# Optimization experiments

Measured on AMD Instinct MI355X. Metric: run time of the kernel, lower is better.

Reference implementation:

```python
import jax, jax.numpy as jnp
import numpy as np

LN_EPS = 1e-5
MASK_FILL = -1e9


def setup_inputs() -> dict:
    key = jax.random.key(0)
    ks = jax.random.split(key, 10)
    B, L, D, H, O, K = 128, 2048, 128, 256, 128, 64
    return {
        "sequence_emb": jax.random.normal(ks[0], (B, L, D), jnp.float32),
        "mask": jax.random.randint(ks[1], (B, L), 0, 2, jnp.int32),
        "target_emb": jax.random.normal(ks[2], (B, D), jnp.float32),
        "pos_table": jax.random.normal(ks[3], (10000, D), jnp.float32) * 0.02,
        "W_imp1": jax.random.normal(ks[4], (3 * D, H), jnp.float32) * (1.0 / np.sqrt(3 * D)),
        "b_imp1": jnp.zeros((H,), jnp.float32),
        "W_imp2": jax.random.normal(ks[5], (H, 1), jnp.float32) * (1.0 / np.sqrt(H)),
        "b_imp2": jnp.zeros((1,), jnp.float32),
        "W_enc1": jax.random.normal(ks[6], (2 * D, H), jnp.float32) * (1.0 / np.sqrt(2 * D)),
        "b_enc1": jnp.zeros((H,), jnp.float32),
        "W_enc2": jax.random.normal(ks[7], (H, O), jnp.float32) * (1.0 / np.sqrt(H)),
        "b_enc2": jnp.zeros((O,), jnp.float32),
        "ln_gamma": jnp.ones((O,), jnp.float32),
        "ln_beta": jnp.zeros((O,), jnp.float32),
        "top_k": K,
    }


def reference(sequence_emb, mask, target_emb, pos_table, W_imp1, b_imp1, W_imp2,
              b_imp2, W_enc1, b_enc1, W_enc2, b_enc2, ln_gamma, ln_beta, top_k):
    B, L, D = sequence_emb.shape
    # position embedding lookup (positions identical across batch -> keep (L,D) and broadcast)
    positions = jnp.minimum(jnp.arange(L), pos_table.shape[0] - 1)
    pos_emb = jnp.broadcast_to(pos_table[positions][None], (B, L, D))
    combined = jnp.concatenate([sequence_emb, pos_emb], axis=-1)          # (B,L,2D)
    tgt = jnp.broadcast_to(target_emb[:, None, :], (B, L, D))
    imp_in = jnp.concatenate([combined, tgt], axis=-1)                    # (B,L,3D)
    # importance MLP -> scalar score per event
    h = jax.nn.relu(imp_in @ W_imp1 + b_imp1)
    scores = (h @ W_imp2 + b_imp2)[..., 0]                                # (B,L)
    scores = jnp.where(mask == 0, MASK_FILL, scores)
    # masked top-k, then gather in chronological (sorted-index) order
    topk_values, topk_indices = jax.lax.top_k(scores, top_k)              # (B,K)
    idx_sorted = jnp.sort(topk_indices, axis=-1)
    sel = jnp.take_along_axis(combined, idx_sorted[..., None], axis=1)    # (B,K,2D)
    encoded = jax.nn.relu(sel @ W_enc1 + b_enc1) @ W_enc2 + b_enc2        # (B,K,O)
    # reorder scores to match sorted index order (torch: gather by argsort of indices)
    order = jnp.argsort(topk_indices, axis=-1)
    topk_scores = jnp.take_along_axis(topk_values, order, axis=-1)
    attn = jax.nn.softmax(topk_scores, axis=-1)                           # (B,K)
    pooled = jnp.einsum('bk,bkd->bd', attn, encoded)                      # (B,O)
    mu = jnp.mean(pooled, axis=-1, keepdims=True)
    var = jnp.var(pooled, axis=-1, keepdims=True)
    return (pooled - mu) * jax.lax.rsqrt(var + LN_EPS) * ln_gamma + ln_beta
```

## Files before the change

### kernel.cpp

```cpp
#include <hip/hip_runtime.h>
#include <hip/hip_bf16.h>

namespace {
constexpr int NB = 128;
constexpr int NL = 2048;
constexpr int ND = 128;
constexpr int NH = 256;
constexpr int NO = 128;
constexpr int NK = 64;
constexpr int MCAP = 192;
constexpr int HTHR = 96;
constexpr int BLOOP = 8;
constexpr float MASK_FILL_F = -1e9f;
constexpr float LN_EPS_F = 1e-5f;
}

typedef __attribute__((ext_vector_type(8))) short bf16x8;
typedef __attribute__((ext_vector_type(4))) float f32x4;

__device__ __forceinline__ unsigned short bf16rne(float x) {
  unsigned u = __float_as_uint(x);
  return (unsigned short)((u + 0x7FFFu + ((u >> 16) & 1u)) >> 16);
}

__global__ __launch_bounds__(256) void k_prep(
    const float* __restrict__ W1, const float* __restrict__ pos,
    const float* __restrict__ tgt, const float* __restrict__ b1,
    unsigned short* __restrict__ W1aT, float* __restrict__ P,
    float* __restrict__ T) {
  const int blk = blockIdx.x, t = threadIdx.x;
  if (blk < ND) {
    W1aT[(size_t)t * ND + blk] = bf16rne(W1[(size_t)blk * NH + t]);
    return;
  }
  int r, w_off, add_bias;
  const float* src;
  float* out;
  if (blk < ND + NL) {
    r = blk - ND; src = pos; out = P; w_off = ND; add_bias = 1;
  } else {
    r = blk - (ND + NL); src = tgt; out = T; w_off = 2 * ND; add_bias = 0;
  }
  __shared__ float row[ND];
  if (t < ND) row[t] = src[(size_t)r * ND + t];
  __syncthreads();
  float acc = add_bias ? b1[t] : 0.0f;
#pragma unroll 8
  for (int d = 0; d < ND; ++d)
    acc = fmaf(row[d], W1[(size_t)(w_off + d) * NH + t], acc);
  out[(size_t)r * NH + t] = acc;
}

__global__ __launch_bounds__(512, 2) void k_scores_mfma(
    const float* __restrict__ seq, const int* __restrict__ mask,
    const unsigned short* __restrict__ W1aT, const float* __restrict__ w2,
    const float* __restrict__ b2, const float* __restrict__ b1,
    const float* __restrict__ T, float* __restrict__ scores) {
  const int l0 = blockIdx.x * 128;
  const int b0 = blockIdx.y * BLOOP;
  const int t = threadIdx.x;
  const int lane = t & 63;
  const int w = t >> 6;
  const int wh = w & 3;
  const int wl = w >> 2;
  const int lh = lane & 15;
  const int kq = lane >> 4;

  __shared__ unsigned short sSeq[2][128 * 128];
  __shared__ float sRed[4][128];

  bf16x8 a[4][4];
#pragma unroll
  for (int ks = 0; ks < 4; ++ks)
#pragma unroll
    for (int mt = 0; mt < 4; ++mt)
      a[ks][mt] = *(const bf16x8*)(
          W1aT + (size_t)(wh * 64 + mt * 16 + lh) * ND + ks * 32 + kq * 8);

  float4 wv[4], b1v[4];
#pragma unroll
  for (int mt = 0; mt < 4; ++mt) {
    wv[mt] = *(const float4*)(w2 + wh * 64 + mt * 16 + kq * 4);
    b1v[mt] = *(const float4*)(b1 + wh * 64 + mt * 16 + kq * 4);
  }
  const float b2v = b2[0];

  ushort4 pf[8];
  auto prefetch = [&](int bb) {
    const float4* g = (const float4*)(seq + ((size_t)bb * NL + l0) * ND);
#pragma unroll
    for (int i = 0; i < 8; ++i) {
      const float4 f = g[t + i * 512];
      pf[i].x = bf16rne(f.x); pf[i].y = bf16rne(f.y);
      pf[i].z = bf16rne(f.z); pf[i].w = bf16rne(f.w);
    }
  };
  auto commit = [&](unsigned short* dst) {
#pragma unroll
    for (int i = 0; i < 8; ++i) {
      const int v = t + i * 512;
      const int row = v >> 5;
      const int c8 = (v & 31) * 8;
      const int off = (row << 8) + (c8 ^ ((row & 15) << 4));
      *(ushort4*)((char*)dst + off) = pf[i];
    }
  };

  prefetch(b0);
  commit((unsigned short*)sSeq[0]);
  __syncthreads();

#pragma unroll 1
  for (int j = 0; j < BLOOP; ++j) {
    const int b = b0 + j;
    unsigned short* cSeq = (unsigned short*)sSeq[j & 1];
    unsigned short* nSeq = (unsigned short*)sSeq[(j & 1) ^ 1];

    if (j + 1 < BLOOP) prefetch(b + 1);

    float4 Tv[4];
#pragma unroll
    for (int mt = 0; mt < 4; ++mt)
      Tv[mt] = *(const float4*)(T + (size_t)b * NH + wh * 64 + mt * 16 + kq * 4);

    f32x4 acc[4][4];
#pragma unroll
    for (int mt = 0; mt < 4; ++mt)
#pragma unroll
      for (int nt = 0; nt < 4; ++nt) acc[mt][nt] = (f32x4){0.f, 0.f, 0.f, 0.f};

#pragma unroll
    for (int ks = 0; ks < 4; ++ks) {
      bf16x8 Bf[4];
#pragma unroll
      for (int nt = 0; nt < 4; ++nt) {
        const int row = wl * 64 + nt * 16 + lh;
        const int off = (row << 8) + (((ks << 6) + (kq << 4)) ^ ((row & 15) << 4));
        Bf[nt] = *(const bf16x8*)((const char*)cSeq + off);
      }
#pragma unroll
      for (int mt = 0; mt < 4; ++mt)
#pragma unroll
        for (int nt = 0; nt < 4; ++nt)
          acc[mt][nt] = __builtin_amdgcn_mfma_f32_16x16x32_bf16(
              a[ks][mt], Bf[nt], acc[mt][nt], 0, 0, 0);
    }
    __syncthreads();
    if (j + 1 < BLOOP) commit(nSeq);

    float p[4] = {0.f, 0.f, 0.f, 0.f};
#pragma unroll
    for (int mt = 0; mt < 4; ++mt) {
#pragma unroll
      for (int nt = 0; nt < 4; ++nt) {
        float z;
        z = acc[mt][nt][0] + Tv[mt].x + b1v[mt].x; p[nt] = fmaf(fmaxf(z, 0.f), wv[mt].x, p[nt]);
        z = acc[mt][nt][1] + Tv[mt].y + b1v[mt].y; p[nt] = fmaf(fmaxf(z, 0.f), wv[mt].y, p[nt]);
        z = acc[mt][nt][2] + Tv[mt].z + b1v[mt].z; p[nt] = fmaf(fmaxf(z, 0.f), wv[mt].z, p[nt]);
        z = acc[mt][nt][3] + Tv[mt].w + b1v[mt].w; p[nt] = fmaf(fmaxf(z, 0.f), wv[mt].w, p[nt]);
      }
    }
#pragma unroll
    for (int nt = 0; nt < 4; ++nt) {
      float v = p[nt];
      v += __shfl_xor(v, 16);
      v += __shfl_xor(v, 32);
      if (lane < 16) sRed[wh][wl * 64 + nt * 16 + lane] = v;
    }
    __syncthreads();
    if (t < 128) {
      const int l = l0 + t;
      float sc = sRed[0][t] + sRed[1][t] + sRed[2][t] + sRed[3][t] + b2v;
      if (mask[(size_t)b * NL + l] == 0) sc = MASK_FILL_F;
      scores[(size_t)b * NL + l] = sc;
    }
  }
}

__global__ __launch_bounds__(256) void k_topM(
    const float* __restrict__ scores, int* __restrict__ cand_idx,
    int* __restrict__ cand_n) {
  const int b = blockIdx.x, t = threadIdx.x;
  __shared__ unsigned hist[4096];
  __shared__ unsigned chunk[256];
  __shared__ int sB;
  __shared__ unsigned sCntHi, sCntB;
  for (int i = t; i < 4096; i += 256) hist[i] = 0;
  if (t == 0) { sCntHi = 0; sCntB = 0; }
  __syncthreads();
  unsigned key[8];
#pragma unroll
  for (int i = 0; i < 8; ++i) {
    unsigned u = __float_as_uint(scores[(size_t)b * NL + t + i * 256]);
    u = (u & 0x80000000u) ? ~u : (u | 0x80000000u);
    key[i] = u;
    atomicAdd(&hist[u >> 20], 1u);
  }
  __syncthreads();
  {
    unsigned s = 0;
#pragma unroll 4
    for (int j = 0; j < 16; ++j) s += hist[t * 16 + j];
    chunk[t] = s;
  }
  __syncthreads();
  if (t == 0) {
    unsigned cum = 0;
    int c = 255;
    for (; c > 0; --c) {
      if (cum + chunk[c] >= (unsigned)HTHR) break;
      cum += chunk[c];
    }
    int bin = c * 16 + 15;
    for (; bin > c * 16; --bin) {
      if (cum + hist[bin] >= (unsigned)HTHR) break;
      cum += hist[bin];
    }
    sB = bin;
  }
  __syncthreads();
  const unsigned B = (unsigned)sB;
#pragma unroll
  for (int i = 0; i < 8; ++i) {
    if ((key[i] >> 20) > B) {
      unsigned pos = atomicAdd(&sCntHi, 1u);
      cand_idx[(size_t)b * MCAP + pos] = t + i * 256;
    }
  }
  __syncthreads();
  const unsigned hi = sCntHi;
#pragma unroll
  for (int i = 0; i < 8; ++i) {
    if ((key[i] >> 20) == B) {
      unsigned pos = atomicAdd(&sCntB, 1u);
      if (hi + pos < (unsigned)MCAP)
        cand_idx[(size_t)b * MCAP + hi + pos] = t + i * 256;
    }
  }
  __syncthreads();
  if (t == 0) {
    unsigned n = hi + sCntB;
    cand_n[b] = (int)(n < (unsigned)MCAP ? n : (unsigned)MCAP);
  }
}

__global__ __launch_bounds__(256) void k_rescore(
    const float* __restrict__ seq, const int* __restrict__ mask,
    const float* __restrict__ W1, const float* __restrict__ w2,
    const float* __restrict__ b2, const float* __restrict__ P,
    const float* __restrict__ T, const int* __restrict__ cand_idx,
    const int* __restrict__ cand_n, float* __restrict__ cscore) {
  const int b = blockIdx.y;
  const int s0 = blockIdx.x * 32;
  const int n = cand_n[b];
  if (s0 >= n) return;
  const int t = threadIdx.x;
  __shared__ float s_seq[32 * 128];
  __shared__ int s_l[32];
  if (t < 32) {
    const int slot = s0 + t;
    s_l[t] = (slot < n) ? cand_idx[(size_t)b * MCAP + slot] : 0;
  }
  __syncthreads();
#pragma unroll
  for (int i = 0; i < 4; ++i) {
    const int v = t + i * 256;
    const int r = v >> 5, c = v & 31;
    ((float4*)s_seq)[r * 32 + c] =
        ((const float4*)(seq + ((size_t)b * NL + s_l[r]) * ND))[c];
  }
  __syncthreads();

  const int hg = t & 63, rg = t >> 6;
  float acc[8][4];
#pragma unroll
  for (int r = 0; r < 8; ++r)
#pragma unroll
    for (int j = 0; j < 4; ++j) acc[r][j] = 0.0f;

  const float4* Wp = (const float4*)W1;
  for (int d0 = 0; d0 < ND; d0 += 4) {
    float4 wq[4];
#pragma unroll
    for (int j = 0; j < 4; ++j) wq[j] = Wp[(size_t)(d0 + j) * (NH / 4) + hg];
#pragma unroll
    for (int r = 0; r < 8; ++r) {
      const float4 s = *(const float4*)&s_seq[(rg * 8 + r) * ND + d0];
      const float sv[4] = {s.x, s.y, s.z, s.w};
#pragma unroll
      for (int j = 0; j < 4; ++j) {
        acc[r][0] = fmaf(sv[j], wq[j].x, acc[r][0]);
        acc[r][1] = fmaf(sv[j], wq[j].y, acc[r][1]);
        acc[r][2] = fmaf(sv[j], wq[j].z, acc[r][2]);
        acc[r][3] = fmaf(sv[j], wq[j].w, acc[r][3]);
      }
    }
  }

  const float4 wv = ((const float4*)w2)[hg];
  const float4 Tv = ((const float4*)(T + (size_t)b * NH))[hg];
  const float b2v = b2[0];
#pragma unroll
  for (int r = 0; r < 8; ++r) {
    const int l = s_l[rg * 8 + r];
    const float4 Pv = ((const float4*)(P + (size_t)l * NH))[hg];
    float z, p = 0.0f;
    z = acc[r][0] + Pv.x + Tv.x; p = fmaf(fmaxf(z, 0.0f), wv.x, p);
    z = acc[r][1] + Pv.y + Tv.y; p = fmaf(fmaxf(z, 0.0f), wv.y, p);
    z = acc[r][2] + Pv.z + Tv.z; p = fmaf(fmaxf(z, 0.0f), wv.z, p);
    z = acc[r][3] + Pv.w + Tv.w; p = fmaf(fmaxf(z, 0.0f), wv.w, p);
#pragma unroll
    for (int off = 32; off >= 1; off >>= 1) p += __shfl_xor(p, off);
    if (hg == 0) {
      float sc = p + b2v;
      if (mask[(size_t)b * NL + l] == 0) sc = MASK_FILL_F;
      cscore[(size_t)b * MCAP + s0 + rg * 8 + r] = sc;
    }
  }
}

__global__ __launch_bounds__(256) void k_select(
    const float* __restrict__ cscore, const int* __restrict__ cand_idx,
    const int* __restrict__ cand_n, int* __restrict__ idx_sorted,
    float* __restrict__ attn) {
  const int b = blockIdx.x, t = threadIdx.x;
  __shared__ unsigned long long key[MCAP];
  __shared__ float val[MCAP];
  __shared__ int sel_l[NK];
  __shared__ float sel_v[NK];
  __shared__ int srt_l[NK];
  __shared__ float srt_v[NK];
  const int n = cand_n[b];
  for (int s = t; s < MCAP; s += 256) {
    unsigned long long kk = 0ull;
    float f = 0.0f;
    if (s < n) {
      f = cscore[(size_t)b * MCAP + s];
      unsigned u = __float_as_uint(f);
      u = (u & 0x80000000u) ? ~u : (u | 0x80000000u);
      const int l = cand_idx[(size_t)b * MCAP + s];
      kk = ((unsigned long long)u << 11) | (unsigned long long)(NL - 1 - l);
    }
    key[s] = kk;
    val[s] = f;
  }
  __syncthreads();

  for (int s = t; s < MCAP; s += 256) {
    if (s < n) {
      const unsigned long long mk = key[s];
      int rank = 0;
      for (int j = 0; j < n; ++j) rank += (key[j] > mk) ? 1 : 0;
      if (rank < NK) {
        sel_l[rank] = (NL - 1) - (int)(mk & 0x7FFull);
        sel_v[rank] = val[s];
      }
    }
  }
  __syncthreads();

  if (t < NK) {
    const int myl = sel_l[t];
    int pos = 0;
#pragma unroll 8
    for (int j = 0; j < NK; ++j) pos += (sel_l[j] < myl) ? 1 : 0;
    srt_l[pos] = myl;
    srt_v[pos] = sel_v[t];
  }
  __syncthreads();

  if (t < 64) {
    const float sc = srt_v[t];
    float m = sc;
#pragma unroll
    for (int off = 32; off >= 1; off >>= 1) m = fmaxf(m, __shfl_xor(m, off));
    const float e = expf(sc - m);
    float s = e;
#pragma unroll
    for (int off = 32; off >= 1; off >>= 1) s += __shfl_xor(s, off);
    attn[(size_t)b * NK + t] = e / s;
    idx_sorted[(size_t)b * NK + t] = srt_l[t];
  }
}

__global__ __launch_bounds__(256) void k_enc1(
    const float* __restrict__ seq, const float* __restrict__ pos,
    const int* __restrict__ idx_sorted, const float* __restrict__ We1,
    const float* __restrict__ be1, float* __restrict__ h1) {
  const int qb = blockIdx.x;
  const int b = blockIdx.y;
  const int t = threadIdx.x;
  __shared__ float s_sel[16 * 256];
  __shared__ int s_idx[16];
  if (t < 16) s_idx[t] = idx_sorted[(size_t)b * NK + qb * 16 + t];
  __syncthreads();
  {
    const int k = t >> 4, q = t & 15;
    const int idx = s_idx[k];
    const float4* sr = (const float4*)(seq + ((size_t)b * NL + idx) * ND);
    const float4* pr = (const float4*)(pos + (size_t)idx * ND);
    float4* d1 = (float4*)&s_sel[k * 256];
    float4* d2 = (float4*)&s_sel[k * 256 + ND];
#pragma unroll
    for (int i = 0; i < 2; ++i) {
      d1[q + i * 16] = sr[q + i * 16];
      d2[q + i * 16] = pr[q + i * 16];
    }
  }
  __syncthreads();

  const int hg = t & 63, rg = t >> 6;
  float acc[4][4];
#pragma unroll
  for (int r = 0; r < 4; ++r)
#pragma unroll
    for (int j = 0; j < 4; ++j) acc[r][j] = 0.0f;

  const float4* Wp = (const float4*)We1;
  for (int d = 0; d < 2 * ND; ++d) {
    const float4 w = Wp[(size_t)d * (NH / 4) + hg];
#pragma unroll
    for (int r = 0; r < 4; ++r) {
      const float s = s_sel[(rg * 4 + r) * 256 + d];
      acc[r][0] = fmaf(s, w.x, acc[r][0]);
      acc[r][1] = fmaf(s, w.y, acc[r][1]);
      acc[r][2] = fmaf(s, w.z, acc[r][2]);
      acc[r][3] = fmaf(s, w.w, acc[r][3]);
    }
  }
  const float4 bev = ((const float4*)be1)[hg];
#pragma unroll
  for (int r = 0; r < 4; ++r) {
    float4 o;
    o.x = fmaxf(acc[r][0] + bev.x, 0.0f);
    o.y = fmaxf(acc[r][1] + bev.y, 0.0f);
    o.z = fmaxf(acc[r][2] + bev.z, 0.0f);
    o.w = fmaxf(acc[r][3] + bev.w, 0.0f);
    ((float4*)(h1 + ((size_t)b * NK + qb * 16 + rg * 4 + r) * NH))[hg] = o;
  }
}

__global__ __launch_bounds__(256) void k_enc2(
    const float* __restrict__ h1, const float* __restrict__ attn,
    const float* __restrict__ We2, const float* __restrict__ be2,
    float* __restrict__ part_g) {
  const int qb = blockIdx.x;
  const int b = blockIdx.y;
  const int t = threadIdx.x;
  __shared__ float s_h1[16 * NH];
  {
    const float4* src = (const float4*)(h1 + ((size_t)b * NK + qb * 16) * NH);
    float4* dst = (float4*)s_h1;
#pragma unroll
    for (int i = 0; i < 4; ++i) dst[t + i * 256] = src[t + i * 256];
  }
  __syncthreads();

  const int og = t & 31;
  const int kg = t >> 5;
  float acc[2][4];
#pragma unroll
  for (int r = 0; r < 2; ++r)
#pragma unroll
    for (int j = 0; j < 4; ++j) acc[r][j] = 0.0f;

  const float4* Wp = (const float4*)We2;
  for (int d = 0; d < NH; ++d) {
    const float4 w = Wp[(size_t)d * (NO / 4) + og];
#pragma unroll
    for (int r = 0; r < 2; ++r) {
      const float s = s_h1[(kg * 2 + r) * NH + d];
      acc[r][0] = fmaf(s, w.x, acc[r][0]);
      acc[r][1] = fmaf(s, w.y, acc[r][1]);
      acc[r][2] = fmaf(s, w.z, acc[r][2]);
      acc[r][3] = fmaf(s, w.w, acc[r][3]);
    }
  }

  const float4 bev = ((const float4*)be2)[og];
  float part[4] = {0.0f, 0.0f, 0.0f, 0.0f};
#pragma unroll
  for (int r = 0; r < 2; ++r) {
    const int k = qb * 16 + kg * 2 + r;
    const float a = attn[(size_t)b * NK + k];
    part[0] = fmaf(a, acc[r][0] + bev.x, part[0]);
    part[1] = fmaf(a, acc[r][1] + bev.y, part[1]);
    part[2] = fmaf(a, acc[r][2] + bev.z, part[2]);
    part[3] = fmaf(a, acc[r][3] + bev.w, part[3]);
  }
#pragma unroll
  for (int j = 0; j < 4; ++j) part[j] += __shfl_xor(part[j], 32);

  __syncthreads();
  float* red = s_h1;
  const int w = t >> 6;
  if ((t & 63) < 32) {
    ((float4*)red)[w * 32 + og] = make_float4(part[0], part[1], part[2], part[3]);
  }
  __syncthreads();
  if (t < NO) {
    part_g[((size_t)qb * NB + b) * NO + t] =
        red[t] + red[NO + t] + red[2 * NO + t] + red[3 * NO + t];
  }
}

__global__ __launch_bounds__(128) void k_ln(
    const float* __restrict__ part_g, const float* __restrict__ gamma,
    const float* __restrict__ beta, float* __restrict__ out) {
  const int b = blockIdx.x, t = threadIdx.x;
  __shared__ float rr[4];
  const float pooled = part_g[((size_t)0 * NB + b) * NO + t] +
                       part_g[((size_t)1 * NB + b) * NO + t] +
                       part_g[((size_t)2 * NB + b) * NO + t] +
                       part_g[((size_t)3 * NB + b) * NO + t];
  float s1 = pooled, s2 = pooled * pooled;
#pragma unroll
  for (int off = 32; off >= 1; off >>= 1) {
    s1 += __shfl_xor(s1, off);
    s2 += __shfl_xor(s2, off);
  }
  if ((t & 63) == 0) { rr[(t >> 6) * 2] = s1; rr[(t >> 6) * 2 + 1] = s2; }
  __syncthreads();
  const float S1 = rr[0] + rr[2];
  const float S2 = rr[1] + rr[3];
  const float mu = S1 / NO;
  const float var = S2 / NO - mu * mu;
  const float rs = rsqrtf(var + LN_EPS_F);
  out[(size_t)b * NO + t] = (pooled - mu) * rs * gamma[t] + beta[t];
}

extern "C" void kernel_launch(void* const* d_in, const int* in_sizes, int n_in,
                              void* d_out, int out_size, void* d_ws, size_t ws_size,
                              hipStream_t stream) {
  (void)in_sizes; (void)n_in; (void)out_size; (void)ws_size;
  const float* seq = (const float*)d_in[0];
  const int* mask = (const int*)d_in[1];
  const float* tgt = (const float*)d_in[2];
  const float* pos = (const float*)d_in[3];
  const float* W1 = (const float*)d_in[4];
  const float* b1 = (const float*)d_in[5];
  const float* w2 = (const float*)d_in[6];
  const float* b2 = (const float*)d_in[7];
  const float* We1 = (const float*)d_in[8];
  const float* be1 = (const float*)d_in[9];
  const float* We2 = (const float*)d_in[10];
  const float* be2 = (const float*)d_in[11];
  const float* gam = (const float*)d_in[12];
  const float* bet = (const float*)d_in[13];
  float* out = (float*)d_out;

  float* P = (float*)d_ws;
  float* T = P + (size_t)NL * NH;
  float* scores = T + (size_t)NB * NH;
  float* attn = scores + (size_t)NB * NL;
  float* h1 = attn + (size_t)NB * NK;
  int* idxs = (int*)(h1 + (size_t)NB * NK * NH);
  unsigned short* w1aT = (unsigned short*)h1;
  int* cand_idx = (int*)(h1 + 16384);
  int* cand_n = cand_idx + (size_t)NB * MCAP;
  float* cscore = (float*)(cand_n + NB);
  float* part_g = scores;

  k_prep<<<ND + NL + NB, 256, 0, stream>>>(W1, pos, tgt, b1, w1aT, P, T);
  k_scores_mfma<<<dim3(NL / 128, NB / BLOOP), 512, 0, stream>>>(
      seq, mask, w1aT, w2, b2, b1, T, scores);
  k_topM<<<NB, 256, 0, stream>>>(scores, cand_idx, cand_n);
  k_rescore<<<dim3(MCAP / 32, NB), 256, 0, stream>>>(seq, mask, W1, w2, b2, P, T,
                                                     cand_idx, cand_n, cscore);
  k_select<<<NB, 256, 0, stream>>>(cscore, cand_idx, cand_n, idxs, attn);
  k_enc1<<<dim3(NK / 16, NB), 256, 0, stream>>>(seq, pos, idxs, We1, be1, h1);
  k_enc2<<<dim3(4, NB), 256, 0, stream>>>(h1, attn, We2, be2, part_g);
  k_ln<<<NB, 128, 0, stream>>>(part_g, gam, bet, out);
}
```

Baseline: 145.3 us.

## Move pos projection into scores kernel, batch prep rows, widen topM block

The position-table projection P, which only the later rescore kernel needs, is moved out of k_prep and computed by extra blocks appended to the k_scores_mfma grid, so it overlaps with the MFMA scoring work instead of running serially before it. The target projection in k_prep now handles 16 rows per block, reusing each W1 load across rows. k_topM switches to 512 threads with 8-bin histogram chunks, halving per-thread work. The costs are extra register pressure in the P blocks sharing the scores kernel's launch bounds, and a longer serial chunk scan in topM thread 0.

```diff
diff --git a/kernel.cpp b/kernel.cpp
--- a/kernel.cpp
+++ b/kernel.cpp
@@ -24,50 +24,75 @@
 }
 
 __global__ __launch_bounds__(256) void k_prep(
-    const float* __restrict__ W1, const float* __restrict__ pos,
-    const float* __restrict__ tgt, const float* __restrict__ b1,
-    unsigned short* __restrict__ W1aT, float* __restrict__ P,
-    float* __restrict__ T) {
+    const float* __restrict__ W1, const float* __restrict__ tgt,
+    unsigned short* __restrict__ W1aT, float* __restrict__ T) {
   const int blk = blockIdx.x, t = threadIdx.x;
   if (blk < ND) {
     W1aT[(size_t)t * ND + blk] = bf16rne(W1[(size_t)blk * NH + t]);
     return;
   }
-  int r, w_off, add_bias;
-  const float* src;
-  float* out;
-  if (blk < ND + NL) {
-    r = blk - ND; src = pos; out = P; w_off = ND; add_bias = 1;
-  } else {
-    r = blk - (ND + NL); src = tgt; out = T; w_off = 2 * ND; add_bias = 0;
-  }
-  __shared__ float row[ND];
-  if (t < ND) row[t] = src[(size_t)r * ND + t];
-  __syncthreads();
-  float acc = add_bias ? b1[t] : 0.0f;
-#pragma unroll 8
-  for (int d = 0; d < ND; ++d)
-    acc = fmaf(row[d], W1[(size_t)(w_off + d) * NH + t], acc);
-  out[(size_t)r * NH + t] = acc;
+  const int r0 = (blk - ND) * 16;
+  __shared__ float srow[16 * ND];
+  for (int i = t; i < 16 * ND; i += 256)
+    srow[i] = tgt[(size_t)(r0 + (i >> 7)) * ND + (i & 127)];
+  __syncthreads();
+  const int h = t;
+  float acc[16];
+#pragma unroll
+  for (int i = 0; i < 16; ++i) acc[i] = 0.0f;
+  for (int d = 0; d < ND; ++d) {
+    const float wv = W1[(size_t)(2 * ND + d) * NH + h];
+#pragma unroll
+    for (int i = 0; i < 16; ++i) acc[i] = fmaf(srow[i * ND + d], wv, acc[i]);
+  }
+#pragma unroll
+  for (int i = 0; i < 16; ++i) T[(size_t)(r0 + i) * NH + h] = acc[i];
 }
 
 __global__ __launch_bounds__(512, 2) void k_scores_mfma(
     const float* __restrict__ seq, const int* __restrict__ mask,
     const unsigned short* __restrict__ W1aT, const float* __restrict__ w2,
     const float* __restrict__ b2, const float* __restrict__ b1,
-    const float* __restrict__ T, float* __restrict__ scores) {
-  const int l0 = blockIdx.x * 128;
-  const int b0 = blockIdx.y * BLOOP;
+    const float* __restrict__ T, const float* __restrict__ pos,
+    const float* __restrict__ W1, float* __restrict__ P,
+    float* __restrict__ scores) {
+  const int blk = blockIdx.x;
   const int t = threadIdx.x;
+
+  __shared__ unsigned short sSeq[2][128 * 128];
+  __shared__ float sRed[4][128];
+
+  if (blk >= 256) {
+    const int l0p = (blk - 256) * 16;
+    float* srow = (float*)sSeq;
+    for (int i = t; i < 16 * ND; i += 512)
+      srow[i] = pos[(size_t)(l0p + (i >> 7)) * ND + (i & 127)];
+    __syncthreads();
+    const int h = t & 255;
+    const int half = t >> 8;
+    float acc[8];
+#pragma unroll
+    for (int r = 0; r < 8; ++r) acc[r] = b1[h];
+    for (int d = 0; d < ND; ++d) {
+      const float wv = W1[(size_t)(ND + d) * NH + h];
+#pragma unroll
+      for (int r = 0; r < 8; ++r)
+        acc[r] = fmaf(srow[(half * 8 + r) * ND + d], wv, acc[r]);
+    }
+#pragma unroll
+    for (int r = 0; r < 8; ++r)
+      P[(size_t)(l0p + half * 8 + r) * NH + h] = acc[r];
+    return;
+  }
+
+  const int l0 = (blk & 15) * 128;
+  const int b0 = (blk >> 4) * BLOOP;
   const int lane = t & 63;
   const int w = t >> 6;
   const int wh = w & 3;
   const int wl = w >> 2;
   const int lh = lane & 15;
   const int kq = lane >> 4;
-
-  __shared__ unsigned short sSeq[2][128 * 128];
-  __shared__ float sRed[4][128];
 
   bf16x8 a[4][4];
 #pragma unroll
@@ -177,21 +202,21 @@
   }
 }
 
-__global__ __launch_bounds__(256) void k_topM(
+__global__ __launch_bounds__(512) void k_topM(
     const float* __restrict__ scores, int* __restrict__ cand_idx,
     int* __restrict__ cand_n) {
   const int b = blockIdx.x, t = threadIdx.x;
   __shared__ unsigned hist[4096];
-  __shared__ unsigned chunk[256];
+  __shared__ unsigned chunk[512];
   __shared__ int sB;
   __shared__ unsigned sCntHi, sCntB;
-  for (int i = t; i < 4096; i += 256) hist[i] = 0;
+  for (int i = t; i < 4096; i += 512) hist[i] = 0;
   if (t == 0) { sCntHi = 0; sCntB = 0; }
   __syncthreads();
-  unsigned key[8];
-#pragma unroll
-  for (int i = 0; i < 8; ++i) {
-    unsigned u = __float_as_uint(scores[(size_t)b * NL + t + i * 256]);
+  unsigned key[4];
+#pragma unroll
+  for (int i = 0; i < 4; ++i) {
+    unsigned u = __float_as_uint(scores[(size_t)b * NL + t + i * 512]);
     u = (u & 0x80000000u) ? ~u : (u | 0x80000000u);
     key[i] = u;
     atomicAdd(&hist[u >> 20], 1u);
@@ -199,20 +224,20 @@
   __syncthreads();
   {
     unsigned s = 0;
-#pragma unroll 4
-    for (int j = 0; j < 16; ++j) s += hist[t * 16 + j];
+#pragma unroll
+    for (int j = 0; j < 8; ++j) s += hist[t * 8 + j];
     chunk[t] = s;
   }
   __syncthreads();
   if (t == 0) {
     unsigned cum = 0;
-    int c = 255;
+    int c = 511;
     for (; c > 0; --c) {
       if (cum + chunk[c] >= (unsigned)HTHR) break;
       cum += chunk[c];
     }
-    int bin = c * 16 + 15;
-    for (; bin > c * 16; --bin) {
+    int bin = c * 8 + 7;
+    for (; bin > c * 8; --bin) {
       if (cum + hist[bin] >= (unsigned)HTHR) break;
       cum += hist[bin];
     }
@@ -221,20 +246,20 @@
   __syncthreads();
   const unsigned B = (unsigned)sB;
 #pragma unroll
-  for (int i = 0; i < 8; ++i) {
+  for (int i = 0; i < 4; ++i) {
     if ((key[i] >> 20) > B) {
       unsigned pos = atomicAdd(&sCntHi, 1u);
-      cand_idx[(size_t)b * MCAP + pos] = t + i * 256;
+      cand_idx[(size_t)b * MCAP + pos] = t + i * 512;
     }
   }
   __syncthreads();
   const unsigned hi = sCntHi;
 #pragma unroll
-  for (int i = 0; i < 8; ++i) {
+  for (int i = 0; i < 4; ++i) {
     if ((key[i] >> 20) == B) {
       unsigned pos = atomicAdd(&sCntB, 1u);
       if (hi + pos < (unsigned)MCAP)
-        cand_idx[(size_t)b * MCAP + hi + pos] = t + i * 256;
+        cand_idx[(size_t)b * MCAP + hi + pos] = t + i * 512;
     }
   }
   __syncthreads();
@@ -561,10 +586,10 @@
   float* cscore = (float*)(cand_n + NB);
   float* part_g = scores;
 
-  k_prep<<<ND + NL + NB, 256, 0, stream>>>(W1, pos, tgt, b1, w1aT, P, T);
-  k_scores_mfma<<<dim3(NL / 128, NB / BLOOP), 512, 0, stream>>>(
-      seq, mask, w1aT, w2, b2, b1, T, scores);
-  k_topM<<<NB, 256, 0, stream>>>(scores, cand_idx, cand_n);
+  k_prep<<<ND + NB / 16, 256, 0, stream>>>(W1, tgt, w1aT, T);
+  k_scores_mfma<<<256 + NL / 16, 512, 0, stream>>>(
+      seq, mask, w1aT, w2, b2, b1, T, pos, W1, P, scores);
+  k_topM<<<NB, 512, 0, stream>>>(scores, cand_idx, cand_n);
   k_rescore<<<dim3(MCAP / 32, NB), 256, 0, stream>>>(seq, mask, W1, w2, b2, P, T,
                                                      cand_idx, cand_n, cscore);
   k_select<<<NB, 256, 0, stream>>>(cscore, cand_idx, cand_n, idxs, attn);
```

Result: slower. 162.5 us (+11.8%).
